# Performance work log

Measured on AMD Instinct MI355X. Metric: run time of the kernel, lower is better.

## Reference

```python
import jax, jax.numpy as jnp
import numpy as np

N_NODES = 100000
N_EDGES = 1600000
N_GRAPHS = 64
IN_DIM = 397


def setup_inputs() -> dict:
    key = jax.random.key(0)
    ks = jax.random.split(key, 16)
    x = jax.random.normal(ks[0], (N_NODES, IN_DIM), dtype=jnp.float32)
    edge_index = jax.random.randint(ks[1], (2, N_EDGES), 0, N_NODES, dtype=jnp.int64)
    batch = jnp.sort(jax.random.randint(ks[2], (N_NODES,), 0, N_GRAPHS, dtype=jnp.int64))

    def lin(k, fan_in, fan_out):
        s = 1.0 / np.sqrt(fan_in)
        return jax.random.uniform(k, (fan_in, fan_out), jnp.float32, -s, s)

    return {
        "x": x, "edge_index": edge_index, "batch": batch,
        "W1": lin(ks[3], IN_DIM, 128), "b1": jnp.zeros((128,), jnp.float32),
        "W2": lin(ks[4], 128, 128),   "b2": jnp.zeros((128,), jnp.float32),
        "W3": lin(ks[5], 128, 64),    "b3": jnp.zeros((64,), jnp.float32),
        "Wh1": lin(ks[6], 64, 32),    "bh1": jnp.zeros((32,), jnp.float32),
        "Wh2": lin(ks[7], 32, 1),     "bh2": jnp.zeros((1,), jnp.float32),
    }


def _gcn_conv(x, src, dst, deg_isqrt, W, b, n_nodes):
    # PyG GCNConv: linear first, then sym-normalized aggregation with self-loops.
    xw = x @ W  # [N, out]
    norm = deg_isqrt[src] * deg_isqrt[dst]  # [E]
    agg = jax.ops.segment_sum(xw[src] * norm[:, None], dst, num_segments=n_nodes)
    # self-loop contribution: deg^{-1/2}[i] * deg^{-1/2}[i] * xw[i]
    agg = agg + xw * (deg_isqrt * deg_isqrt)[:, None]
    return agg + b


def reference(x, edge_index, batch, W1, b1, W2, b2, W3, b3, Wh1, bh1, Wh2, bh2):
    n_nodes = x.shape[0]
    src, dst = edge_index[0], edge_index[1]
    # degree after adding self-loops (edge weight 1), counted at destination
    deg = jax.ops.segment_sum(jnp.ones_like(src, dtype=x.dtype), dst,
                              num_segments=n_nodes) + 1.0
    deg_isqrt = jax.lax.rsqrt(deg)

    h = jax.nn.relu(_gcn_conv(x, src, dst, deg_isqrt, W1, b1, n_nodes))
    # dropout p=0.2 -> identity in eval
    h = jax.nn.relu(_gcn_conv(h, src, dst, deg_isqrt, W2, b2, n_nodes))
    h = jax.nn.relu(_gcn_conv(h, src, dst, deg_isqrt, W3, b3, n_nodes))

    # global max pool over graphs in the batch
    g = jax.ops.segment_max(h, batch, num_segments=N_GRAPHS)  # [G, 64]

    # MLP head (Dropout(0.3) identity in eval)
    g = jax.nn.relu(g @ Wh1 + bh1)
    out = g @ Wh2 + bh2  # [G, 1]
    return out.squeeze(-1)
```

## Files before the change

kernel.cpp:

```cpp
#include <hip/hip_runtime.h>
#include <hip/hip_bf16.h>
#include <hip/hip_fp16.h>


typedef float f4u __attribute__((ext_vector_type(4), aligned(4)));
typedef unsigned short u16;
typedef u16 u16x8 __attribute__((ext_vector_type(8)));
typedef short bf16x8 __attribute__((ext_vector_type(8)));
typedef float f32x4 __attribute__((ext_vector_type(4)));
typedef _Float16 f16;
typedef f16 f16x8 __attribute__((ext_vector_type(8)));

__device__ __forceinline__ u16 bf16_rne(float f) {
    unsigned u = __float_as_uint(f);
    return (u16)((u + 0x7FFF + ((u >> 16) & 1)) >> 16);
}
__device__ __forceinline__ float bf16_f(u16 h) {
    return __uint_as_float(((unsigned)h) << 16);
}

__global__ void deg_count_kernel(const int* __restrict__ ei, int* __restrict__ cnt, int E) {
    int e = blockIdx.x * 256 + threadIdx.x;
    if (e < E) atomicAdd(&cnt[ei[E + e]], 1);
}

__global__ void deg_fin_kernel(const int* __restrict__ cnt, float* __restrict__ disq, int N) {
    int i = blockIdx.x * 256 + threadIdx.x;
    if (i < N) disq[i] = rsqrtf((float)cnt[i] + 1.0f);
}

__global__ void scan_pass1(const int* __restrict__ cnt, int* __restrict__ bsum, int N) {
    __shared__ int s[256];
    int t = threadIdx.x;
    int base = blockIdx.x * 1024 + t * 4;
    int sum = 0;
    #pragma unroll
    for (int j = 0; j < 4; ++j) { int idx = base + j; if (idx < N) sum += cnt[idx]; }
    s[t] = sum; __syncthreads();
    for (int off = 128; off; off >>= 1) {
        if (t < off) s[t] += s[t + off];
        __syncthreads();
    }
    if (t == 0) bsum[blockIdx.x] = s[0];
}

__global__ void scan_pass2(const int* __restrict__ bsum, int* __restrict__ boff,
                           int nchunks, int* __restrict__ rp, int N, int E) {
    __shared__ int s[256];
    int t = threadIdx.x;
    int v = (t < nchunks) ? bsum[t] : 0;
    s[t] = v; __syncthreads();
    for (int off = 1; off < 256; off <<= 1) {
        int x = (t >= off) ? s[t - off] : 0;
        __syncthreads();
        s[t] += x;
        __syncthreads();
    }
    boff[t] = s[t] - v;
    if (t == 0) rp[N] = E;
}

__global__ void scan_pass3(const int* __restrict__ cnt, const int* __restrict__ boff,
                           int* __restrict__ rp, int N) {
    __shared__ int s[256];
    int t = threadIdx.x;
    int base = blockIdx.x * 1024 + t * 4;
    int v[4]; int sum = 0;
    #pragma unroll
    for (int j = 0; j < 4; ++j) { int idx = base + j; v[j] = (idx < N) ? cnt[idx] : 0; sum += v[j]; }
    s[t] = sum; __syncthreads();
    for (int off = 1; off < 256; off <<= 1) {
        int x = (t >= off) ? s[t - off] : 0;
        __syncthreads();
        s[t] += x;
        __syncthreads();
    }
    int ex = s[t] - sum + boff[blockIdx.x];
    #pragma unroll
    for (int j = 0; j < 4; ++j) { int idx = base + j; if (idx < N) { rp[idx] = ex; ex += v[j]; } }
}

__global__ void scatter_kernel(const int* __restrict__ ei, const float* __restrict__ disq,
                               const int* __restrict__ rp, int* __restrict__ fill,
                               int2* __restrict__ esw, int E) {
    int e = blockIdx.x * 256 + threadIdx.x;
    if (e >= E) return;
    int s = ei[e];
    int d = ei[E + e];
    int pos = rp[d] + atomicAdd(&fill[d], 1);
    int2 p; p.x = s; p.y = __float_as_int(disq[s] * disq[d]);
    esw[pos] = p;
}

template <int BN>
__global__ void cvtw_kernel(const float* __restrict__ W, u16* __restrict__ Wfhi,
                            u16* __restrict__ Wflo, int K, int KP) {
    constexpr int FC = BN / 16;
    int idx = blockIdx.x * 256 + threadIdx.x;
    if (idx >= KP * BN) return;
    int j = idx & 7;
    int s = (idx >> 3) & 63;
    int tf = idx >> 9;
    int fc = tf % FC;
    int t = tf / FC;
    int c = fc * 16 + (s & 15);
    int k = t * 32 + ((s >> 4) & 3) * 8 + j;
    float v = (k < K) ? W[(long)k * BN + c] : 0.f;
    u16 h = bf16_rne(v);
    Wfhi[idx] = h;
    Wflo[idx] = bf16_rne(v - bf16_f(h));
}

template <int BN, int AMODE>
__global__ __launch_bounds__(512) void mfma_gemm(
    const float* __restrict__ Af, const f16* __restrict__ Ah16,
    const u16* __restrict__ Wfhi, const u16* __restrict__ Wflo,
    f16* __restrict__ Xh, int N, int K, int KP)
{
    constexpr int FC = BN / 16;
    constexpr int PLANE = BN * 32;
    __shared__ u16 Wlds[2][2 * PLANE];
    const int tid = threadIdx.x;
    const int w = tid >> 6;
    const int l = tid & 63;
    const int l15 = l & 15;
    const int g = l >> 4;
    const int koff = g * 8;
    const long base = (long)blockIdx.x * 128;
    const long arow = base + w * 16 + l15;
    const bool rowOK = (arow < N);
    const int bro = l * 8;
    const int T = KP / 32;

    f32x4 acc[FC];
    #pragma unroll
    for (int j = 0; j < FC; ++j) acc[j] = (f32x4){0.f, 0.f, 0.f, 0.f};

    auto stageW = [&](int t, int buf) {
        if (BN == 128 || tid < PLANE / 8) {
            const u16* gph = Wfhi + (long)t * PLANE + tid * 8;
            const u16* gpl = Wflo + (long)t * PLANE + tid * 8;
            __builtin_amdgcn_global_load_lds(
                (const __attribute__((address_space(1))) void*)gph,
                (__attribute__((address_space(3))) void*)((char*)&Wlds[buf][0] + w * 1024), 16, 0, 0);
            __builtin_amdgcn_global_load_lds(
                (const __attribute__((address_space(1))) void*)gpl,
                (__attribute__((address_space(3))) void*)((char*)&Wlds[buf][PLANE] + w * 1024), 16, 0, 0);
        }
    };
    auto loadRawF = [&](int t, f4u& ra, f4u& rb) {
        ra = (f4u){0.f, 0.f, 0.f, 0.f};
        rb = (f4u){0.f, 0.f, 0.f, 0.f};
        if (t < T) {
            int k0 = t * 32;
            int rem = K - (k0 + koff);
            if (rowOK && rem > 0) {
                const float* ap = &Af[arow * (long)K + k0 + koff];
                if (rem >= 8) {
                    ra = *(const f4u*)ap;
                    rb = *(const f4u*)(ap + 4);
                } else {
                    float f[8];
                    #pragma unroll
                    for (int j = 0; j < 8; ++j) f[j] = (j < rem) ? ap[j] : 0.f;
                    ra = (f4u){f[0], f[1], f[2], f[3]};
                    rb = (f4u){f[4], f[5], f[6], f[7]};
                }
            }
        }
    };
    auto convF = [&](const f4u& ra, const f4u& rb, bf16x8& ah, bf16x8& al) {
        float f[8] = {ra.x, ra.y, ra.z, ra.w, rb.x, rb.y, rb.z, rb.w};
        u16x8 hv, lv;
        #pragma unroll
        for (int j = 0; j < 8; ++j) {
            u16 h = bf16_rne(f[j]);
            hv[j] = h;
            lv[j] = bf16_rne(f[j] - bf16_f(h));
        }
        ah = __builtin_bit_cast(bf16x8, hv);
        al = __builtin_bit_cast(bf16x8, lv);
    };
    auto loadRawH = [&](int t, u16x8& q) {
        q = (u16x8)0;
        if (t < T && rowOK) {
            const int k0 = t * 32;
            q = *(const u16x8*)&Ah16[arow * (long)K + k0 + koff];
        }
    };
    auto convH = [&](const u16x8& q, bf16x8& ah, bf16x8& al) {
        f16x8 v = __builtin_bit_cast(f16x8, q);
        u16x8 hv, lv;
        #pragma unroll
        for (int j = 0; j < 8; ++j) {
            float f = (float)v[j];
            u16 h = bf16_rne(f);
            hv[j] = h;
            lv[j] = bf16_rne(f - bf16_f(h));
        }
        ah = __builtin_bit_cast(bf16x8, hv);
        al = __builtin_bit_cast(bf16x8, lv);
    };
    auto domfma = [&](const bf16x8& ah, const bf16x8& al, int buf) {
        #pragma unroll
        for (int fc = 0; fc < FC; ++fc) {
            bf16x8 bh = *(const bf16x8*)&Wlds[buf][fc * 512 + bro];
            bf16x8 bl = *(const bf16x8*)&Wlds[buf][PLANE + fc * 512 + bro];
            acc[fc] = __builtin_amdgcn_mfma_f32_16x16x32_bf16(ah, bh, acc[fc], 0, 0, 0);
            acc[fc] = __builtin_amdgcn_mfma_f32_16x16x32_bf16(al, bh, acc[fc], 0, 0, 0);
            acc[fc] = __builtin_amdgcn_mfma_f32_16x16x32_bf16(ah, bl, acc[fc], 0, 0, 0);
        }
    };

    f4u r0a, r0b, r1a, r1b;
    u16x8 q0, q1;
    bf16x8 a0h, a0l, a1h, a1l;

    stageW(0, 0);
    if constexpr (AMODE == 0) {
        loadRawF(0, r0a, r0b);
        loadRawF(1, r1a, r1b);
        convF(r0a, r0b, a0h, a0l);
    } else {
        loadRawH(0, q0);
        loadRawH(1, q1);
        convH(q0, a0h, a0l);
    }
    __syncthreads();

    for (int t = 0; t < T; t += 2) {
        if (t + 1 < T) stageW(t + 1, 1);
        if constexpr (AMODE == 0) loadRawF(t + 2, r0a, r0b);
        else                      loadRawH(t + 2, q0);
        domfma(a0h, a0l, 0);
        if constexpr (AMODE == 0) convF(r1a, r1b, a1h, a1l);
        else                      convH(q1, a1h, a1l);
        __syncthreads();
        if (t + 1 < T) {
            if (t + 2 < T) stageW(t + 2, 0);
            if constexpr (AMODE == 0) loadRawF(t + 3, r1a, r1b);
            else                      loadRawH(t + 3, q1);
            domfma(a1h, a1l, 1);
            if constexpr (AMODE == 0) convF(r0a, r0b, a0h, a0l);
            else                      convH(q0, a0h, a0l);
            __syncthreads();
        }
    }
    #pragma unroll
    for (int fc = 0; fc < FC; ++fc) {
        int col = fc * 16 + l15;
        #pragma unroll
        for (int reg = 0; reg < 4; ++reg) {
            long row = base + w * 16 + g * 4 + reg;
            if (row < N) Xh[row * BN + col] = (f16)acc[fc][reg];
        }
    }
}

template <int C>
__global__ __launch_bounds__(256) void agg_kernel(
    const f16* __restrict__ xh, const float* __restrict__ disq,
    const int* __restrict__ rp, const int2* __restrict__ esw,
    const float* __restrict__ bias, f16* __restrict__ hout, int N)
{
    int i = blockIdx.x * 4 + (threadIdx.x >> 6);
    if (i >= N) return;
    int lane = threadIdx.x & 63;
    int e0 = rp[i], e1 = rp[i + 1];
    constexpr int LPE = C / 8;
    constexpr int EPW = 64 / LPE;
    int sub = lane / LPE;
    int col = lane % LPE;
    const f16x8* x8 = (const f16x8*)xh;

    float a0[8], a1[8];
    #pragma unroll
    for (int j = 0; j < 8; ++j) { a0[j] = 0.f; a1[j] = 0.f; }

    int e = e0 + sub;
    for (; e + EPW < e1; e += 2 * EPW) {
        int2 p0 = esw[e];
        int2 p1 = esw[e + EPW];
        f16x8 v0 = x8[(long)p0.x * LPE + col];
        f16x8 v1 = x8[(long)p1.x * LPE + col];
        float w0 = __int_as_float(p0.y), w1 = __int_as_float(p1.y);
        #pragma unroll
        for (int j = 0; j < 8; ++j) {
            a0[j] += (float)v0[j] * w0;
            a1[j] += (float)v1[j] * w1;
        }
    }
    for (; e < e1; e += EPW) {
        int2 p0 = esw[e];
        f16x8 v0 = x8[(long)p0.x * LPE + col];
        float w0 = __int_as_float(p0.y);
        #pragma unroll
        for (int j = 0; j < 8; ++j) a0[j] += (float)v0[j] * w0;
    }
    #pragma unroll
    for (int j = 0; j < 8; ++j) a0[j] += a1[j];
    #pragma unroll
    for (int m = LPE; m < 64; m <<= 1) {
        #pragma unroll
        for (int j = 0; j < 8; ++j) a0[j] += __shfl_xor(a0[j], m, 64);
    }
    if (sub == 0) {
        float ds = disq[i];
        float ws = ds * ds;
        f16x8 v = x8[(long)i * LPE + col];
        const float* bp = bias + col * 8;
        float4 b0 = *(const float4*)bp;
        float4 b1 = *(const float4*)(bp + 4);
        float bb[8] = {b0.x, b0.y, b0.z, b0.w, b1.x, b1.y, b1.z, b1.w};
        f16x8 o;
        #pragma unroll
        for (int j = 0; j < 8; ++j)
            o[j] = (f16)fmaxf(a0[j] + (float)v[j] * ws + bb[j], 0.f);
        *(f16x8*)&hout[(long)i * C + col * 8] = o;
    }
}

__global__ __launch_bounds__(256) void pool_kernel(
    const f16* __restrict__ h, const int* __restrict__ batch,
    float* __restrict__ g, int N)
{
    int c = threadIdx.x & 63;
    int slot = threadIdx.x >> 6;
    int base = blockIdx.x * 512;
    int end = base + 512; if (end > N) end = N;
    int cur = -1; float m = 0.f;
    for (int n = base + slot; n < end; n += 4) {
        int b = batch[n];
        float v = (float)h[(long)n * 64 + c];
        if (b != cur) {
            if (cur >= 0) atomicMax((int*)&g[cur * 64 + c], __float_as_int(m));
            cur = b; m = v;
        } else {
            m = fmaxf(m, v);
        }
    }
    if (cur >= 0) atomicMax((int*)&g[cur * 64 + c], __float_as_int(m));
}

__global__ void head_kernel(const float* __restrict__ g, const float* __restrict__ Wh1,
                            const float* __restrict__ bh1, const float* __restrict__ Wh2,
                            const float* __restrict__ bh2, float* __restrict__ out, int G) {
    int r = threadIdx.x;
    if (r >= G) return;
    float hid[32];
    #pragma unroll
    for (int j = 0; j < 32; ++j) {
        float s = bh1[j];
        for (int k = 0; k < 64; ++k) s += g[r * 64 + k] * Wh1[k * 32 + j];
        hid[j] = fmaxf(s, 0.f);
    }
    float o = bh2[0];
    #pragma unroll
    for (int j = 0; j < 32; ++j) o += hid[j] * Wh2[j];
    out[r] = o;
}

extern "C" void kernel_launch(void* const* d_in, const int* in_sizes, int n_in,
                              void* d_out, int out_size, void* d_ws, size_t ws_size,
                              hipStream_t stream) {
    const float* x   = (const float*)d_in[0];
    const int*   ei  = (const int*)d_in[1];
    const int*   bat = (const int*)d_in[2];
    const float* W1  = (const float*)d_in[3];
    const float* b1  = (const float*)d_in[4];
    const float* W2  = (const float*)d_in[5];
    const float* b2  = (const float*)d_in[6];
    const float* W3  = (const float*)d_in[7];
    const float* b3  = (const float*)d_in[8];
    const float* Wh1 = (const float*)d_in[9];
    const float* bh1 = (const float*)d_in[10];
    const float* Wh2 = (const float*)d_in[11];
    const float* bh2 = (const float*)d_in[12];
    float* out = (float*)d_out;

    const int N = in_sizes[2];
    const int E = in_sizes[1] / 2;
    const int K1 = in_sizes[0] / N;
    const int G = out_size;
    const int KP1 = ((K1 + 31) / 32) * 32;

    char* wsp = (char*)d_ws;
    size_t off = 0;
    auto alloc = [&](size_t bytes) -> void* {
        void* p = wsp + off;
        off = (off + bytes + 255) & ~(size_t)255;
        return p;
    };
    int*   cnt   = (int*)alloc((size_t)N * 4);
    float* disq  = (float*)alloc((size_t)N * 4);
    int*   rp    = (int*)alloc((size_t)(N + 1) * 4);
    int*   bsum  = (int*)alloc(256 * 4);
    int*   boff  = (int*)alloc(256 * 4);
    int2*  esw   = (int2*)alloc((size_t)E * 8);
    u16*   Wf1hi = (u16*)alloc((size_t)KP1 * 128 * 2);
    u16*   Wf1lo = (u16*)alloc((size_t)KP1 * 128 * 2);
    u16*   Wf2hi = (u16*)alloc((size_t)128 * 128 * 2);
    u16*   Wf2lo = (u16*)alloc((size_t)128 * 128 * 2);
    u16*   Wf3hi = (u16*)alloc((size_t)128 * 64 * 2);
    u16*   Wf3lo = (u16*)alloc((size_t)128 * 64 * 2);
    f16*   Xh    = (f16*)alloc((size_t)N * 128 * 2);
    f16*   Hh    = (f16*)alloc((size_t)N * 128 * 2);
    float* g     = (float*)alloc((size_t)G * 64 * 4);

    const int nchunks = (N + 1023) / 1024;

    (void)hipMemsetAsync(cnt, 0, (size_t)N * 4, stream);
    deg_count_kernel<<<(E + 255) / 256, 256, 0, stream>>>(ei, cnt, E);
    deg_fin_kernel<<<(N + 255) / 256, 256, 0, stream>>>(cnt, disq, N);
    scan_pass1<<<nchunks, 256, 0, stream>>>(cnt, bsum, N);
    scan_pass2<<<1, 256, 0, stream>>>(bsum, boff, nchunks, rp, N, E);
    scan_pass3<<<nchunks, 256, 0, stream>>>(cnt, boff, rp, N);
    (void)hipMemsetAsync(cnt, 0, (size_t)N * 4, stream);
    scatter_kernel<<<(E + 255) / 256, 256, 0, stream>>>(ei, disq, rp, cnt, esw, E);

    cvtw_kernel<128><<<(KP1 * 128 + 255) / 256, 256, 0, stream>>>(W1, Wf1hi, Wf1lo, K1, KP1);
    cvtw_kernel<128><<<(128 * 128 + 255) / 256, 256, 0, stream>>>(W2, Wf2hi, Wf2lo, 128, 128);
    cvtw_kernel<64><<<(128 * 64 + 255) / 256, 256, 0, stream>>>(W3, Wf3hi, Wf3lo, 128, 128);

    int gblocks = (N + 127) / 128;
    int ablocks = (N + 3) / 4;
    mfma_gemm<128, 0><<<gblocks, 512, 0, stream>>>(x, nullptr, Wf1hi, Wf1lo, Xh, N, K1, KP1);
    agg_kernel<128><<<ablocks, 256, 0, stream>>>(Xh, disq, rp, esw, b1, Hh, N);
    mfma_gemm<128, 1><<<gblocks, 512, 0, stream>>>(nullptr, Hh, Wf2hi, Wf2lo, Xh, N, 128, 128);
    agg_kernel<128><<<ablocks, 256, 0, stream>>>(Xh, disq, rp, esw, b2, Hh, N);
    mfma_gemm<64, 1><<<gblocks, 512, 0, stream>>>(nullptr, Hh, Wf3hi, Wf3lo, Xh, N, 128, 128);
    agg_kernel<64><<<ablocks, 256, 0, stream>>>(Xh, disq, rp, esw, b3, Hh, N);
    (void)hipMemsetAsync(g, 0, (size_t)G * 64 * 4, stream);
    pool_kernel<<<(N + 511) / 512, 256, 0, stream>>>(Hh, bat, g, N);
    head_kernel<<<1, 64, 0, stream>>>(g, Wh1, bh1, Wh2, bh2, out, G);
}
```

Measured before the change: 477.5 us.

## Replace block barriers with partial vmcnt waits and branchless padded A loads

Replaces __syncthreads in the GEMM main loop with explicit s_waitcnt vmcnt(N) plus s_barrier, so the prefetched A register loads can stay in flight across the barrier while only the LDS weight staging is waited on. To make A loads unconditional, out-of-range rows are clamped to row 0 and zeroed by a multiply mask. The ragged K tail of x is copied into a zero-padded N×32 buffer by a new kernel. The extra kernel adds about 12.8MB of traffic, and the hand-counted vmcnt values depend on the compiler's issue order of loads.

```diff
diff --git a/kernel.cpp b/kernel.cpp
--- a/kernel.cpp
+++ b/kernel.cpp
@@ -90,6 +90,15 @@
     int pos = rp[d] + atomicAdd(&fill[d], 1);
     int2 p; p.x = s; p.y = __float_as_int(disq[s] * disq[d]);
     esw[pos] = p;
+}
+
+__global__ void pad_tail_kernel(const float* __restrict__ x, float* __restrict__ xt,
+                                int N, int K, int KP) {
+    int idx = blockIdx.x * 256 + threadIdx.x;
+    if (idx >= N * 32) return;
+    int i = idx >> 5, j = idx & 31;
+    int k = KP - 32 + j;
+    xt[idx] = (k < K) ? x[(long)i * K + k] : 0.f;
 }
 
 template <int BN>
@@ -113,7 +122,8 @@
 
 template <int BN, int AMODE>
 __global__ __launch_bounds__(512) void mfma_gemm(
-    const float* __restrict__ Af, const f16* __restrict__ Ah16,
+    const float* __restrict__ Af, const float* __restrict__ Xt,
+    const f16* __restrict__ Ah16,
     const u16* __restrict__ Wfhi, const u16* __restrict__ Wflo,
     f16* __restrict__ Xh, int N, int K, int KP)
 {
@@ -129,6 +139,8 @@
     const long base = (long)blockIdx.x * 128;
     const long arow = base + w * 16 + l15;
     const bool rowOK = (arow < N);
+    const long arow_c = rowOK ? arow : 0;
+    const float keepm = rowOK ? 1.f : 0.f;
     const int bro = l * 8;
     const int T = KP / 32;
 
@@ -147,26 +159,27 @@
                 (const __attribute__((address_space(1))) void*)gpl,
                 (__attribute__((address_space(3))) void*)((char*)&Wlds[buf][PLANE] + w * 1024), 16, 0, 0);
         }
+        asm volatile("" ::: "memory");
+    };
+    auto syncw = [&](bool keepA) {
+        if (keepA) {
+            if constexpr (AMODE == 0) asm volatile("s_waitcnt vmcnt(2)" ::: "memory");
+            else                      asm volatile("s_waitcnt vmcnt(1)" ::: "memory");
+        } else {
+            asm volatile("s_waitcnt vmcnt(0)" ::: "memory");
+        }
+        __builtin_amdgcn_s_barrier();
+        asm volatile("" ::: "memory");
     };
     auto loadRawF = [&](int t, f4u& ra, f4u& rb) {
-        ra = (f4u){0.f, 0.f, 0.f, 0.f};
-        rb = (f4u){0.f, 0.f, 0.f, 0.f};
         if (t < T) {
-            int k0 = t * 32;
-            int rem = K - (k0 + koff);
-            if (rowOK && rem > 0) {
-                const float* ap = &Af[arow * (long)K + k0 + koff];
-                if (rem >= 8) {
-                    ra = *(const f4u*)ap;
-                    rb = *(const f4u*)(ap + 4);
-                } else {
-                    float f[8];
-                    #pragma unroll
-                    for (int j = 0; j < 8; ++j) f[j] = (j < rem) ? ap[j] : 0.f;
-                    ra = (f4u){f[0], f[1], f[2], f[3]};
-                    rb = (f4u){f[4], f[5], f[6], f[7]};
-                }
-            }
+            const float* ap = (t == T - 1) ? &Xt[arow_c * 32 + koff]
+                                           : &Af[arow_c * (long)K + t * 32 + koff];
+            ra = *(const f4u*)ap;
+            rb = *(const f4u*)(ap + 4);
+        } else {
+            ra = (f4u){0.f, 0.f, 0.f, 0.f};
+            rb = (f4u){0.f, 0.f, 0.f, 0.f};
         }
     };
     auto convF = [&](const f4u& ra, const f4u& rb, bf16x8& ah, bf16x8& al) {
@@ -174,26 +187,24 @@
         u16x8 hv, lv;
         #pragma unroll
         for (int j = 0; j < 8; ++j) {
-            u16 h = bf16_rne(f[j]);
+            float fv = f[j] * keepm;
+            u16 h = bf16_rne(fv);
             hv[j] = h;
-            lv[j] = bf16_rne(f[j] - bf16_f(h));
+            lv[j] = bf16_rne(fv - bf16_f(h));
         }
         ah = __builtin_bit_cast(bf16x8, hv);
         al = __builtin_bit_cast(bf16x8, lv);
     };
     auto loadRawH = [&](int t, u16x8& q) {
-        q = (u16x8)0;
-        if (t < T && rowOK) {
-            const int k0 = t * 32;
-            q = *(const u16x8*)&Ah16[arow * (long)K + k0 + koff];
-        }
+        if (t < T) q = *(const u16x8*)&Ah16[arow_c * (long)K + t * 32 + koff];
+        else       q = (u16x8)0;
     };
     auto convH = [&](const u16x8& q, bf16x8& ah, bf16x8& al) {
         f16x8 v = __builtin_bit_cast(f16x8, q);
         u16x8 hv, lv;
         #pragma unroll
         for (int j = 0; j < 8; ++j) {
-            float f = (float)v[j];
+            float f = (float)v[j] * keepm;
             u16 h = bf16_rne(f);
             hv[j] = h;
             lv[j] = bf16_rne(f - bf16_f(h));
@@ -226,7 +237,7 @@
         loadRawH(1, q1);
         convH(q0, a0h, a0l);
     }
-    __syncthreads();
+    syncw(true);
 
     for (int t = 0; t < T; t += 2) {
         if (t + 1 < T) stageW(t + 1, 1);
@@ -235,7 +246,7 @@
         domfma(a0h, a0l, 0);
         if constexpr (AMODE == 0) convF(r1a, r1b, a1h, a1l);
         else                      convH(q1, a1h, a1l);
-        __syncthreads();
+        syncw(t + 2 < T);
         if (t + 1 < T) {
             if (t + 2 < T) stageW(t + 2, 0);
             if constexpr (AMODE == 0) loadRawF(t + 3, r1a, r1b);
@@ -243,7 +254,7 @@
             domfma(a1h, a1l, 1);
             if constexpr (AMODE == 0) convF(r0a, r0b, a0h, a0l);
             else                      convH(q0, a0h, a0l);
-            __syncthreads();
+            syncw(t + 3 < T);
         }
     }
     #pragma unroll
@@ -403,6 +414,7 @@
     u16*   Wf2lo = (u16*)alloc((size_t)128 * 128 * 2);
     u16*   Wf3hi = (u16*)alloc((size_t)128 * 64 * 2);
     u16*   Wf3lo = (u16*)alloc((size_t)128 * 64 * 2);
+    float* xt    = (float*)alloc((size_t)N * 32 * 4);
     f16*   Xh    = (f16*)alloc((size_t)N * 128 * 2);
     f16*   Hh    = (f16*)alloc((size_t)N * 128 * 2);
     float* g     = (float*)alloc((size_t)G * 64 * 4);
@@ -421,14 +433,15 @@
     cvtw_kernel<128><<<(KP1 * 128 + 255) / 256, 256, 0, stream>>>(W1, Wf1hi, Wf1lo, K1, KP1);
     cvtw_kernel<128><<<(128 * 128 + 255) / 256, 256, 0, stream>>>(W2, Wf2hi, Wf2lo, 128, 128);
     cvtw_kernel<64><<<(128 * 64 + 255) / 256, 256, 0, stream>>>(W3, Wf3hi, Wf3lo, 128, 128);
+    pad_tail_kernel<<<((N * 32) + 255) / 256, 256, 0, stream>>>(x, xt, N, K1, KP1);
 
     int gblocks = (N + 127) / 128;
     int ablocks = (N + 3) / 4;
-    mfma_gemm<128, 0><<<gblocks, 512, 0, stream>>>(x, nullptr, Wf1hi, Wf1lo, Xh, N, K1, KP1);
+    mfma_gemm<128, 0><<<gblocks, 512, 0, stream>>>(x, xt, nullptr, Wf1hi, Wf1lo, Xh, N, K1, KP1);
     agg_kernel<128><<<ablocks, 256, 0, stream>>>(Xh, disq, rp, esw, b1, Hh, N);
-    mfma_gemm<128, 1><<<gblocks, 512, 0, stream>>>(nullptr, Hh, Wf2hi, Wf2lo, Xh, N, 128, 128);
+    mfma_gemm<128, 1><<<gblocks, 512, 0, stream>>>(nullptr, nullptr, Hh, Wf2hi, Wf2lo, Xh, N, 128, 128);
     agg_kernel<128><<<ablocks, 256, 0, stream>>>(Xh, disq, rp, esw, b2, Hh, N);
-    mfma_gemm<64, 1><<<gblocks, 512, 0, stream>>>(nullptr, Hh, Wf3hi, Wf3lo, Xh, N, 128, 128);
+    mfma_gemm<64, 1><<<gblocks, 512, 0, stream>>>(nullptr, nullptr, Hh, Wf3hi, Wf3lo, Xh, N, 128, 128);
     agg_kernel<64><<<ablocks, 256, 0, stream>>>(Xh, disq, rp, esw, b3, Hh, N);
     (void)hipMemsetAsync(g, 0, (size_t)G * 64 * 4, stream);
     pool_kernel<<<(N + 511) / 512, 256, 0, stream>>>(Hh, bat, g, N);
```

Result: slower. 495.3 us (+3.7%).
